# Kernel tuning notes

Measured on AMD Instinct MI355X. Metric: run time of the kernel, lower is better.

The kernel has to match this reference:

```python
import jax, jax.numpy as jnp
import numpy as np

B, C, H, W = 32, 512, 112, 112
RC = 32          # reduction_channels = 512 // 16
CPG = C // RC    # channels per group = 16
K, STRIDE, PAD = 3, 2, 1


def setup_inputs() -> dict:
    key = jax.random.key(0)
    ks = jax.random.split(key, 7)
    x = jax.random.normal(ks[0], (B, C, H, W), dtype=jnp.float32)
    # grouped conv weights: OIHW with I = in_channels // groups
    theta_w = jax.random.normal(ks[1], (RC, CPG, K, K), dtype=jnp.float32) * 0.05
    theta_b = jax.random.normal(ks[2], (RC,), dtype=jnp.float32) * 0.05
    phi_w = jax.random.normal(ks[3], (RC, CPG, K, K), dtype=jnp.float32) * 0.05
    phi_b = jax.random.normal(ks[4], (RC,), dtype=jnp.float32) * 0.05
    fc_w = jax.random.normal(ks[5], (RC, CPG, 1, 1), dtype=jnp.float32) * 0.05
    fc_b = jax.random.normal(ks[6], (RC,), dtype=jnp.float32) * 0.05
    return {"x": x, "theta_w": theta_w, "theta_b": theta_b,
            "phi_w": phi_w, "phi_b": phi_b, "fc_w": fc_w, "fc_b": fc_b}


def _gconv(x, w, b, stride, pad):
    groups = x.shape[1] // w.shape[1]
    y = jax.lax.conv_general_dilated(
        x, w, window_strides=(stride, stride),
        padding=[(pad, pad), (pad, pad)],
        dimension_numbers=("NCHW", "OIHW", "NCHW"),
        feature_group_count=groups)
    return y + b[None, :, None, None]


def reference(x, theta_w, theta_b, phi_w, phi_b, fc_w, fc_b):
    b = x.shape[0]
    theta = _gconv(x, theta_w, theta_b, STRIDE, PAD)          # [B,RC,56,56]
    rc = theta.shape[1]
    theta = theta.reshape(b, rc, -1)                          # [B,RC,S]
    phi = _gconv(x, phi_w, phi_b, STRIDE, PAD).reshape(b, rc, -1)  # [B,RC,S]
    # global average pool + grouped 1x1 fc (stride irrelevant on 1x1 input)
    gap = jnp.mean(x, axis=(2, 3))                            # [B,C]
    g = jnp.einsum("bgk,gk->bg", gap.reshape(b, rc, -1), fc_w[:, :, 0, 0]) + fc_b  # [B,RC]
    # channel-channel attention: theta @ phi^T -> softmax -> @ g
    mat = jnp.einsum("bcs,bds->bcd", theta, phi)              # [B,RC,RC]
    mat = jax.nn.softmax(mat, axis=-1)
    out = jnp.einsum("bcd,bd->bc", mat, g)                    # [B,RC]
    return out[:, :, None, None]                              # [B,RC,1,1]
```

## Files before the change

### kernel.cpp

```cpp
#include <hip/hip_runtime.h>

#define BATCH 32
#define CIN   512
#define HH    112
#define WW    112
#define RC    32
#define CPG   16
#define HO    56
#define WO    56
#define TY    4
#define NTILE 14
#define SPT   (TY*WO)
#define XROWS 9
#define XW    120
#define TSP   228
#define HW    (HH*WW)

#define WS_MAT 0
#define WS_GAP (BATCH*NTILE*RC*RC)

__device__ __forceinline__ float4 ldx(const float* p, bool pred) {
    float4 v = make_float4(0.f, 0.f, 0.f, 0.f);
    if (pred) v = *(const float4*)p;
    return v;
}

__global__ __launch_bounds__(256, 2)
void conv_gram_kernel(const float* __restrict__ x,
                      const float* __restrict__ thw, const float* __restrict__ thb,
                      const float* __restrict__ phw, const float* __restrict__ phb,
                      const float* __restrict__ fcw,
                      float* __restrict__ matpart, float* __restrict__ gpart)
{
    const int t   = blockIdx.x;
    const int b   = blockIdx.y;
    const int tid = threadIdx.x;

    __shared__ __align__(16) float xs[2][XROWS*XW];
    __shared__ __align__(16) float th_s[RC*TSP];
    __shared__ __align__(16) float ph_s[RC*TSP];
    __shared__ float g_red[4*RC];

    for (int r = tid; r < XROWS; r += 256) {
        #pragma unroll
        for (int k = 0; k < 4; ++k) {
            xs[0][r*XW + k] = 0.f;       xs[1][r*XW + k] = 0.f;
            xs[0][r*XW + 116 + k] = 0.f; xs[1][r*XW + 116 + k] = 0.f;
        }
    }

    const bool sact = tid < 252;
    const int  srow = (4*tid) / WW;
    const int  scol = (4*tid) % WW;
    const bool oobz = (t == 0) && (srow == 0);
    const bool ldp  = sact && !oobz;
    const bool gapv = sact && (srow >= 1);
    const float* xbase = x + (size_t)b*CIN*HW + (long)(8*t - 1 + srow)*WW + scol;
    const int  sdst = srow*XW + 4 + scol;

    const bool cact = tid < SPT;
    const int  ry   = tid / WO;
    const int  ox   = tid - ry*WO;
    const int  cbase = (2*ry)*XW + 3 + 2*ox;

    float4 v0 = ldx(xbase, ldp);
    if (sact) *(float4*)(&xs[0][sdst]) = v0;
    float gcur = gapv ? (v0.x + v0.y + v0.z + v0.w) * fcw[0] : 0.f;
    float4 va = ldx(xbase + (size_t)1*HW, ldp);
    float4 vb = ldx(xbase + (size_t)2*HW, ldp);

    for (int g = 0; g < RC; ++g) {
        float tacc = thb[g];
        float pacc = phb[g];
        #pragma unroll 4
        for (int i = 0; i < CPG; ++i) {
            const int ch = g*CPG + i;
            float4 vn = make_float4(0.f, 0.f, 0.f, 0.f);
            if (ch + 3 < CIN) vn = ldx(xbase + (size_t)(ch + 3)*HW, ldp);

            __syncthreads();

            if (cact) {
                const float* xr = &xs[ch & 1][cbase];
                const float* wt = thw + ch*9;
                const float* wp = phw + ch*9;
                const float a0 = xr[0],      a1 = xr[1],      a2 = xr[2];
                const float b0 = xr[XW],     b1 = xr[XW+1],   b2 = xr[XW+2];
                const float c0 = xr[2*XW],   c1 = xr[2*XW+1], c2 = xr[2*XW+2];
                tacc = fmaf(a0, wt[0], tacc); pacc = fmaf(a0, wp[0], pacc);
                tacc = fmaf(a1, wt[1], tacc); pacc = fmaf(a1, wp[1], pacc);
                tacc = fmaf(a2, wt[2], tacc); pacc = fmaf(a2, wp[2], pacc);
                tacc = fmaf(b0, wt[3], tacc); pacc = fmaf(b0, wp[3], pacc);
                tacc = fmaf(b1, wt[4], tacc); pacc = fmaf(b1, wp[4], pacc);
                tacc = fmaf(b2, wt[5], tacc); pacc = fmaf(b2, wp[5], pacc);
                tacc = fmaf(c0, wt[6], tacc); pacc = fmaf(c0, wp[6], pacc);
                tacc = fmaf(c1, wt[7], tacc); pacc = fmaf(c1, wp[7], pacc);
                tacc = fmaf(c2, wt[8], tacc); pacc = fmaf(c2, wp[8], pacc);
            }

            if (i == CPG - 1) {
                if (cact) { th_s[g*TSP + tid] = tacc; ph_s[g*TSP + tid] = pacc; }
                float r = gcur;
                #pragma unroll
                for (int off = 32; off; off >>= 1) r += __shfl_down(r, off);
                if ((tid & 63) == 0) g_red[(tid >> 6)*RC + g] = r;
                gcur = 0.f;
            }

            if (ch + 1 < CIN) {
                if (sact) *(float4*)(&xs[(ch + 1) & 1][sdst]) = va;
                if (gapv) gcur = fmaf(va.x + va.y + va.z + va.w, fcw[ch + 1], gcur);
                va = vb; vb = vn;
            }
        }
    }

    __syncthreads();

    {
        const int c  = tid >> 3;
        const int dq = tid & 7;
        const float* tr = th_s + c*TSP;
        const float* p0 = ph_s + dq*TSP;
        float a0 = 0.f, a1 = 0.f, a2 = 0.f, a3 = 0.f;
        for (int s = 0; s < SPT; s += 4) {
            const float4 tv = *(const float4*)(tr + s);
            const float4 q0 = *(const float4*)(p0 + s);
            const float4 q1 = *(const float4*)(p0 + 8*TSP + s);
            const float4 q2 = *(const float4*)(p0 + 16*TSP + s);
            const float4 q3 = *(const float4*)(p0 + 24*TSP + s);
            a0 += tv.x*q0.x + tv.y*q0.y + tv.z*q0.z + tv.w*q0.w;
            a1 += tv.x*q1.x + tv.y*q1.y + tv.z*q1.z + tv.w*q1.w;
            a2 += tv.x*q2.x + tv.y*q2.y + tv.z*q2.z + tv.w*q2.w;
            a3 += tv.x*q3.x + tv.y*q3.y + tv.z*q3.z + tv.w*q3.w;
        }
        float* mp = matpart + ((size_t)b*NTILE + t)*(RC*RC) + c*RC + dq;
        mp[0]  = a0;
        mp[8]  = a1;
        mp[16] = a2;
        mp[24] = a3;
    }

    if (tid < RC) {
        const float s = g_red[tid] + g_red[RC + tid] + g_red[2*RC + tid] + g_red[3*RC + tid];
        gpart[((size_t)b*NTILE + t)*RC + tid] = s;
    }
}

__global__ __launch_bounds__(256)
void final_kernel(const float* __restrict__ matpart, const float* __restrict__ gpart,
                  const float* __restrict__ fcb, float* __restrict__ out)
{
    const int b   = blockIdx.x;
    const int tid = threadIdx.x;
    __shared__ float m_s[RC*33];
    __shared__ float g_s[RC];

    for (int idx = tid; idx < RC*RC; idx += 256) {
        float s = 0.f;
        const float* mp = matpart + (size_t)b*NTILE*RC*RC + idx;
        #pragma unroll
        for (int tt = 0; tt < NTILE; ++tt) s += mp[tt*RC*RC];
        m_s[(idx >> 5)*33 + (idx & 31)] = s;
    }
    if (tid < RC) {
        float s = 0.f;
        const float* gp = gpart + (size_t)b*NTILE*RC + tid;
        #pragma unroll
        for (int tt = 0; tt < NTILE; ++tt) s += gp[tt*RC];
        g_s[tid] = fcb[tid] + s * (1.0f/(float)HW);
    }
    __syncthreads();
    if (tid < RC) {
        const float* row = m_s + tid*33;
        float m = -1e30f;
        for (int d = 0; d < RC; ++d) m = fmaxf(m, row[d]);
        float se = 0.f, num = 0.f;
        for (int d = 0; d < RC; ++d) {
            const float e = expf(row[d] - m);
            se  += e;
            num += e * g_s[d];
        }
        out[b*RC + tid] = num / se;
    }
}

extern "C" void kernel_launch(void* const* d_in, const int* in_sizes, int n_in,
                              void* d_out, int out_size, void* d_ws, size_t ws_size,
                              hipStream_t stream)
{
    const float* x   = (const float*)d_in[0];
    const float* thw = (const float*)d_in[1];
    const float* thb = (const float*)d_in[2];
    const float* phw = (const float*)d_in[3];
    const float* phb = (const float*)d_in[4];
    const float* fcw = (const float*)d_in[5];
    const float* fcb = (const float*)d_in[6];
    float* out = (float*)d_out;
    float* ws  = (float*)d_ws;

    float* matpart = ws + WS_MAT;
    float* gpart   = ws + WS_GAP;

    conv_gram_kernel<<<dim3(NTILE, BATCH), 256, 0, stream>>>(
        x, thw, thb, phw, phb, fcw, matpart, gpart);
    final_kernel<<<BATCH, 256, 0, stream>>>(matpart, gpart, fcb, out);
}
```

Baseline: 1.129 ms.

## Split conv over channel chunks and separate gram into its own kernel

```diff
diff --git a/kernel.cpp b/kernel.cpp
--- a/kernel.cpp
+++ b/kernel.cpp
@@ -15,14 +15,173 @@
 #define XW    120
 #define TSP   228
 #define HW    (HH*WW)
+#define SHO   (HO*WO)
+#define NCHUNK 8
+#define GPC   (RC/NCHUNK)
+#define CPC   (GPC*CPG)
 
 #define WS_MAT 0
 #define WS_GAP (BATCH*NTILE*RC*RC)
+#define WS_TH  (WS_GAP + BATCH*NTILE*RC)
+#define WS_PH  (WS_TH + (size_t)BATCH*RC*SHO)
+#define WS_NEED_FLOATS (WS_PH + (size_t)BATCH*RC*SHO)
+#define WS_NEED_BYTES  (WS_NEED_FLOATS * 4)
+#define WS_FUSED_BYTES ((size_t)(WS_GAP + BATCH*NTILE*RC) * 4)
 
 __device__ __forceinline__ float4 ldx(const float* p, bool pred) {
     float4 v = make_float4(0.f, 0.f, 0.f, 0.f);
     if (pred) v = *(const float4*)p;
     return v;
+}
+
+__global__ __launch_bounds__(256, 4)
+void conv_kernel(const float* __restrict__ x,
+                 const float* __restrict__ thw, const float* __restrict__ thb,
+                 const float* __restrict__ phw, const float* __restrict__ phb,
+                 const float* __restrict__ fcw,
+                 float* __restrict__ theta, float* __restrict__ phi,
+                 float* __restrict__ gpart)
+{
+    const int t   = blockIdx.x;
+    const int ck  = blockIdx.y;
+    const int b   = blockIdx.z;
+    const int tid = threadIdx.x;
+    const int c0  = ck * CPC;
+
+    __shared__ __align__(16) float xs[2][XROWS*XW];
+    __shared__ float g_red[4*GPC];
+
+    for (int r = tid; r < XROWS; r += 256) {
+        #pragma unroll
+        for (int k = 0; k < 4; ++k) {
+            xs[0][r*XW + k] = 0.f;       xs[1][r*XW + k] = 0.f;
+            xs[0][r*XW + 116 + k] = 0.f; xs[1][r*XW + 116 + k] = 0.f;
+        }
+    }
+
+    const bool sact = tid < 252;
+    const int  srow = (4*tid) / WW;
+    const int  scol = (4*tid) % WW;
+    const bool oobz = (t == 0) && (srow == 0);
+    const bool ldp  = sact && !oobz;
+    const bool gapv = sact && (srow >= 1);
+    const float* xbase = x + (size_t)b*CIN*HW + (size_t)c0*HW
+                           + (long)(8*t - 1 + srow)*WW + scol;
+    const int  sdst = srow*XW + 4 + scol;
+
+    const bool cact = tid < SPT;
+    const int  ry   = tid / WO;
+    const int  ox   = tid - ry*WO;
+    const int  cbase = (2*ry)*XW + 3 + 2*ox;
+
+    float4 v0 = ldx(xbase, ldp);
+    if (sact) *(float4*)(&xs[0][sdst]) = v0;
+    float gcur = gapv ? (v0.x + v0.y + v0.z + v0.w) * fcw[c0] : 0.f;
+    float4 va = ldx(xbase + (size_t)1*HW, ldp);
+    float4 vb = ldx(xbase + (size_t)2*HW, ldp);
+
+    for (int gl = 0; gl < GPC; ++gl) {
+        const int g = ck*GPC + gl;
+        float tacc = thb[g];
+        float pacc = phb[g];
+        #pragma unroll 4
+        for (int i = 0; i < CPG; ++i) {
+            const int cl = gl*CPG + i;
+            const int ch = c0 + cl;
+            float4 vn = make_float4(0.f, 0.f, 0.f, 0.f);
+            if (cl + 3 < CPC) vn = ldx(xbase + (size_t)(cl + 3)*HW, ldp);
+
+            __syncthreads();
+
+            if (cact) {
+                const float* xr = &xs[cl & 1][cbase];
+                const float* wt = thw + ch*9;
+                const float* wp = phw + ch*9;
+                const float a0 = xr[0],      a1 = xr[1],      a2 = xr[2];
+                const float b0 = xr[XW],     b1 = xr[XW+1],   b2 = xr[XW+2];
+                const float c0v = xr[2*XW],  c1 = xr[2*XW+1], c2 = xr[2*XW+2];
+                tacc = fmaf(a0, wt[0], tacc); pacc = fmaf(a0, wp[0], pacc);
+                tacc = fmaf(a1, wt[1], tacc); pacc = fmaf(a1, wp[1], pacc);
+                tacc = fmaf(a2, wt[2], tacc); pacc = fmaf(a2, wp[2], pacc);
+                tacc = fmaf(b0, wt[3], tacc); pacc = fmaf(b0, wp[3], pacc);
+                tacc = fmaf(b1, wt[4], tacc); pacc = fmaf(b1, wp[4], pacc);
+                tacc = fmaf(b2, wt[5], tacc); pacc = fmaf(b2, wp[5], pacc);
+                tacc = fmaf(c0v, wt[6], tacc); pacc = fmaf(c0v, wp[6], pacc);
+                tacc = fmaf(c1, wt[7], tacc); pacc = fmaf(c1, wp[7], pacc);
+                tacc = fmaf(c2, wt[8], tacc); pacc = fmaf(c2, wp[8], pacc);
+            }
+
+            if (i == CPG - 1) {
+                if (cact) {
+                    const size_t o = ((size_t)b*RC + g)*SHO + (size_t)t*SPT + tid;
+                    theta[o] = tacc;
+                    phi[o]   = pacc;
+                }
+                float r = gcur;
+                #pragma unroll
+                for (int off = 32; off; off >>= 1) r += __shfl_down(r, off);
+                if ((tid & 63) == 0) g_red[(tid >> 6)*GPC + gl] = r;
+                gcur = 0.f;
+            }
+
+            if (cl + 1 < CPC) {
+                if (sact) *(float4*)(&xs[(cl + 1) & 1][sdst]) = va;
+                if (gapv) gcur = fmaf(va.x + va.y + va.z + va.w, fcw[ch + 1], gcur);
+                va = vb; vb = vn;
+            }
+        }
+    }
+
+    __syncthreads();
+    if (tid < GPC) {
+        const float s = g_red[tid] + g_red[GPC + tid]
+                      + g_red[2*GPC + tid] + g_red[3*GPC + tid];
+        gpart[((size_t)b*NTILE + t)*RC + ck*GPC + tid] = s;
+    }
+}
+
+__global__ __launch_bounds__(256, 2)
+void gram_kernel(const float* __restrict__ theta, const float* __restrict__ phi,
+                 float* __restrict__ matpart)
+{
+    const int t   = blockIdx.x;
+    const int b   = blockIdx.y;
+    const int tid = threadIdx.x;
+
+    __shared__ __align__(16) float th_s[RC*TSP];
+    __shared__ __align__(16) float ph_s[RC*TSP];
+
+    const int s0 = t*SPT;
+    for (int idx = tid; idx < RC*(SPT/4); idx += 256) {
+        const int g  = idx / (SPT/4);
+        const int s4 = idx - g*(SPT/4);
+        const size_t o = ((size_t)b*RC + g)*SHO + s0 + 4*s4;
+        *(float4*)(&th_s[g*TSP + 4*s4]) = *(const float4*)(theta + o);
+        *(float4*)(&ph_s[g*TSP + 4*s4]) = *(const float4*)(phi + o);
+    }
+    __syncthreads();
+
+    const int c  = tid >> 3;
+    const int dq = tid & 7;
+    const float* tr = th_s + c*TSP;
+    const float* p0 = ph_s + dq*TSP;
+    float a0 = 0.f, a1 = 0.f, a2 = 0.f, a3 = 0.f;
+    for (int s = 0; s < SPT; s += 4) {
+        const float4 tv = *(const float4*)(tr + s);
+        const float4 q0 = *(const float4*)(p0 + s);
+        const float4 q1 = *(const float4*)(p0 + 8*TSP + s);
+        const float4 q2 = *(const float4*)(p0 + 16*TSP + s);
+        const float4 q3 = *(const float4*)(p0 + 24*TSP + s);
+        a0 += tv.x*q0.x + tv.y*q0.y + tv.z*q0.z + tv.w*q0.w;
+        a1 += tv.x*q1.x + tv.y*q1.y + tv.z*q1.z + tv.w*q1.w;
+        a2 += tv.x*q2.x + tv.y*q2.y + tv.z*q2.z + tv.w*q2.w;
+        a3 += tv.x*q3.x + tv.y*q3.y + tv.z*q3.z + tv.w*q3.w;
+    }
+    float* mp = matpart + ((size_t)b*NTILE + t)*(RC*RC) + c*RC + dq;
+    mp[0]  = a0;
+    mp[8]  = a1;
+    mp[16] = a2;
+    mp[24] = a3;
 }
 
 __global__ __launch_bounds__(256, 2)
@@ -202,7 +361,15 @@
     float* matpart = ws + WS_MAT;
     float* gpart   = ws + WS_GAP;
 
-    conv_gram_kernel<<<dim3(NTILE, BATCH), 256, 0, stream>>>(
-        x, thw, thb, phw, phb, fcw, matpart, gpart);
+    if (ws_size >= (size_t)WS_NEED_BYTES) {
+        float* theta = ws + WS_TH;
+        float* phi   = ws + WS_PH;
+        conv_kernel<<<dim3(NTILE, NCHUNK, BATCH), 256, 0, stream>>>(
+            x, thw, thb, phw, phb, fcw, theta, phi, gpart);
+        gram_kernel<<<dim3(NTILE, BATCH), 256, 0, stream>>>(theta, phi, matpart);
+    } else {
+        conv_gram_kernel<<<dim3(NTILE, BATCH), 256, 0, stream>>>(
+            x, thw, thb, phw, phb, fcw, matpart, gpart);
+    }
     final_kernel<<<BATCH, 256, 0, stream>>>(matpart, gpart, fcb, out);
 }
```

Measured after the change: 1.069 ms. 5.4% less time.
